# Kernel optimization log

Measured on AMD Instinct MI355X. Metric: run time of the kernel, lower is better.

## Reference

```python
import jax, jax.numpy as jnp
import numpy as np

N_NODES = 50000
N_EDGES = 800000
IN_FEATS = 128
OUT_FEATS = 128
HEADS = 2
EW_DIMS = 2
NEG_SLOPE = 0.2


def setup_inputs() -> dict:
    key = jax.random.key(0)
    ks = jax.random.split(key, 8)
    feat = jax.random.normal(ks[0], (N_NODES, IN_FEATS), dtype=jnp.float32)
    e_w = jax.random.uniform(ks[1], (N_EDGES, EW_DIMS), dtype=jnp.float32)
    src = jax.random.randint(ks[2], (N_EDGES,), 0, N_NODES)
    dst = jax.random.randint(ks[3], (N_EDGES,), 0, N_NODES)
    # Learned params: per-head fc weight, attn vectors (xavier-ish scale)
    s = 1.0 / np.sqrt(IN_FEATS)
    W = jax.random.normal(ks[4], (HEADS, OUT_FEATS, IN_FEATS), dtype=jnp.float32) * s
    attn_l = jax.random.normal(ks[5], (HEADS, OUT_FEATS), dtype=jnp.float32) * s
    attn_r = jax.random.normal(ks[6], (HEADS, OUT_FEATS), dtype=jnp.float32) * s
    attn_ew = jax.random.normal(ks[7], (HEADS, EW_DIMS), dtype=jnp.float32)
    return {"feat": feat, "e_w": e_w, "src": src, "dst": dst,
            "W": W, "attn_l": attn_l, "attn_r": attn_r, "attn_ew": attn_ew}


def reference(feat, e_w, src, dst, W, attn_l, attn_r, attn_ew):
    N = feat.shape[0]
    # per-head projection: [N, H, O]
    ft = jnp.einsum('nf,hof->nho', feat, W)
    el = jnp.einsum('nho,ho->nh', ft, attn_l)           # [N, H]
    er = jnp.einsum('nho,ho->nh', ft, attn_r)           # [N, H]
    ew = jnp.einsum('ed,hd->eh', e_w, attn_ew)          # [E, H]
    # u_add_v + edge-weight attention + leaky_relu
    e = jax.nn.leaky_relu(el[src] + er[dst] + ew, NEG_SLOPE)  # [E, H]
    # edge_softmax grouped by destination node (numerically stable)
    emax = jax.ops.segment_max(e, dst, num_segments=N)
    emax = jnp.where(jnp.isfinite(emax), emax, 0.0)
    ee = jnp.exp(e - emax[dst])
    denom = jax.ops.segment_sum(ee, dst, num_segments=N)
    a = ee / jnp.where(denom[dst] > 0, denom[dst], 1.0)       # [E, H]
    # u_mul_e / sum aggregation: [N, H, O]
    m = ft[src] * a[:, :, None]
    rst = jax.ops.segment_sum(m, dst, num_segments=N)
    # residual (Identity since in_feats == out_feats) + elu, then cat heads
    rst = jax.nn.elu(rst + feat[:, None, :])
    return rst.reshape(N, -1)
```

## Files before the change

### kernel.cpp

```cpp
#include <hip/hip_runtime.h>
#include <hip/hip_bf16.h>
#include <math.h>

#define NNODES 50000
#define NEDGES 800000
#define INF 128
#define OUTF 128
#define HEADS 2
#define NEG_SLOPE 0.2f

#define CAP 32
#define OVFCAP 32768

__device__ __forceinline__ unsigned short f2bf(float f) {
    unsigned u = __float_as_uint(f);
    unsigned r = (u + 0x7FFFu + ((u >> 16) & 1u)) >> 16;
    return (unsigned short)r;
}
__device__ __forceinline__ float bf2f(unsigned short b) {
    return __uint_as_float((unsigned)b << 16);
}

typedef __attribute__((ext_vector_type(8))) short frag_ab;
typedef __attribute__((ext_vector_type(4))) float frag_cd;

#define APITCH 136

__global__ void init_kernel(int* cursor, int* ovfcnt, int N) {
    int i = blockIdx.x * 256 + threadIdx.x;
    if (i < N) cursor[i] = 0;
    if (i == 0) *ovfcnt = 0;
}

__global__ __launch_bounds__(256) void gemm_mfma(const float* __restrict__ feat,
                                                 const float* __restrict__ W,
                                                 const float* __restrict__ attn_l,
                                                 const float* __restrict__ attn_r,
                                                 unsigned short* __restrict__ ftb,
                                                 float* __restrict__ elp,
                                                 float* __restrict__ erp,
                                                 int N) {
    __shared__ unsigned short Asl[64 * APITCH];
    __shared__ unsigned short Bsl[64 * APITCH];
    const int t = threadIdx.x;
    const int n0 = blockIdx.x * 64;
    const int w = t >> 6, lane = t & 63;
    const int m16 = lane & 15, quad = lane >> 4;

#pragma unroll
    for (int i = 0; i < 8; ++i) {
        int q = t + i * 256;
        int r = q >> 5;
        int c4 = q & 31;
        int gn = n0 + r;
        float4 g = (gn < N) ? *(const float4*)(feat + (size_t)gn * INF + c4 * 4)
                            : make_float4(0.f, 0.f, 0.f, 0.f);
        ushort4 v; v.x = f2bf(g.x); v.y = f2bf(g.y); v.z = f2bf(g.z); v.w = f2bf(g.w);
        *(ushort4*)(&Asl[r * APITCH + c4 * 4]) = v;
    }

    const int arow = w * 16 + m16;

    for (int jt = 0; jt < 4; ++jt) {
        __syncthreads();
#pragma unroll
        for (int i = 0; i < 8; ++i) {
            int q = t + i * 256;
            int r = q >> 5;
            int c4 = q & 31;
            float4 g = *(const float4*)(W + (size_t)(jt * 64 + r) * INF + c4 * 4);
            ushort4 v; v.x = f2bf(g.x); v.y = f2bf(g.y); v.z = f2bf(g.z); v.w = f2bf(g.w);
            *(ushort4*)(&Bsl[r * APITCH + c4 * 4]) = v;
        }
        __syncthreads();

        frag_cd acc[4];
#pragma unroll
        for (int nt = 0; nt < 4; ++nt) acc[nt] = frag_cd{0.f, 0.f, 0.f, 0.f};

#pragma unroll
        for (int kc = 0; kc < 4; ++kc) {
            frag_ab af = *(frag_ab*)(&Asl[arow * APITCH + kc * 32 + quad * 8]);
#pragma unroll
            for (int nt = 0; nt < 4; ++nt) {
                frag_ab bf = *(frag_ab*)(&Bsl[(nt * 16 + m16) * APITCH + kc * 32 + quad * 8]);
                acc[nt] = __builtin_amdgcn_mfma_f32_16x16x32_bf16(af, bf, acc[nt], 0, 0, 0);
            }
        }

        float pl[4] = {0.f, 0.f, 0.f, 0.f};
        float pr[4] = {0.f, 0.f, 0.f, 0.f};
#pragma unroll
        for (int nt = 0; nt < 4; ++nt) {
            int gj = jt * 64 + nt * 16 + m16;
            float a_l = attn_l[gj];
            float a_r = attn_r[gj];
#pragma unroll
            for (int reg = 0; reg < 4; ++reg) {
                float val = acc[nt][reg];
                pl[reg] += val * a_l;
                pr[reg] += val * a_r;
                int gm = n0 + w * 16 + quad * 4 + reg;
                if (gm < N)
                    ftb[(size_t)gm * 256 + gj] = f2bf(val);
            }
        }
#pragma unroll
        for (int m = 1; m < 16; m <<= 1) {
#pragma unroll
            for (int reg = 0; reg < 4; ++reg) {
                pl[reg] += __shfl_xor(pl[reg], m, 64);
                pr[reg] += __shfl_xor(pr[reg], m, 64);
            }
        }
        if (m16 == 0) {
#pragma unroll
            for (int reg = 0; reg < 4; ++reg) {
                int gm = n0 + w * 16 + quad * 4 + reg;
                if (gm < N) {
                    elp[(size_t)gm * 4 + jt] = pl[reg];
                    erp[(size_t)gm * 4 + jt] = pr[reg];
                }
            }
        }
    }
}

__global__ void edge_fused(const float* __restrict__ elp, const float* __restrict__ erp,
                           const float* __restrict__ e_w, const int* __restrict__ src,
                           const int* __restrict__ dst, const float* __restrict__ attn_ew,
                           int* __restrict__ cursor, int* __restrict__ ovfcnt,
                           uint2* __restrict__ edata, float4* __restrict__ ovf,
                           int E) {
    int e = blockIdx.x * 256 + threadIdx.x;
    if (e >= E) return;
    int s = src[e], d = dst[e];
    float2 ew2 = *(const float2*)(e_w + (size_t)e * 2);
    float4 elv = *(const float4*)(elp + (size_t)s * 4);
    float4 erv = *(const float4*)(erp + (size_t)d * 4);
    float v0 = (elv.x + elv.y) + (erv.x + erv.y) + ew2.x * attn_ew[0] + ew2.y * attn_ew[1];
    float v1 = (elv.z + elv.w) + (erv.z + erv.w) + ew2.x * attn_ew[2] + ew2.y * attn_ew[3];
    v0 = v0 >= 0.f ? v0 : NEG_SLOPE * v0;
    v1 = v1 >= 0.f ? v1 : NEG_SLOPE * v1;
    float ee0 = __expf(v0);
    float ee1 = __expf(v1);
    int pos = atomicAdd(cursor + d, 1);
    if (pos < CAP) {
        unsigned pk = ((unsigned)f2bf(ee1) << 16) | (unsigned)f2bf(ee0);
        edata[(size_t)d * CAP + pos] = make_uint2((unsigned)s, pk);
    } else {
        int o = atomicAdd(ovfcnt, 1);
        if (o < OVFCAP)
            ovf[o] = make_float4(__int_as_float(d), __int_as_float(s), ee0, ee1);
    }
}

__global__ __launch_bounds__(256) void aggregate(const unsigned short* __restrict__ ftb,
                                                 const float* __restrict__ feat,
                                                 const uint2* __restrict__ edata,
                                                 const int* __restrict__ cursor,
                                                 const int* __restrict__ ovfcnt,
                                                 const float4* __restrict__ ovf,
                                                 float* __restrict__ out, int N) {
    const int t = threadIdx.x;
    const int w = t >> 6, l = t & 63;
    const int n = blockIdx.x * 4 + w;
    if (n >= N) return;
    const int c0 = 4 * l;
    const int h = l >> 5;
    const int cnt = cursor[n];
    const int cmain = cnt < CAP ? cnt : CAP;
    const uint2* eb = edata + (size_t)n * CAP;

    float4 acc = make_float4(0.f, 0.f, 0.f, 0.f);
    float dn = 0.f;
#pragma unroll 4
    for (int i = 0; i < cmain; ++i) {
        uint2 rec = eb[i];
        int s = (int)rec.x;
        float a = bf2f((unsigned short)(h ? (rec.y >> 16) : (rec.y & 0xFFFFu)));
        dn += a;
        ushort4 v = *(const ushort4*)(ftb + (size_t)s * 256 + c0);
        acc.x += a * bf2f(v.x);
        acc.y += a * bf2f(v.y);
        acc.z += a * bf2f(v.z);
        acc.w += a * bf2f(v.w);
    }
    if (cnt > CAP) {
        int no = *ovfcnt; if (no > OVFCAP) no = OVFCAP;
        for (int i = 0; i < no; ++i) {
            float4 ov = ovf[i];
            if (__float_as_int(ov.x) == n) {
                int s = __float_as_int(ov.y);
                float a = h ? ov.w : ov.z;
                dn += a;
                ushort4 v = *(const ushort4*)(ftb + (size_t)s * 256 + c0);
                acc.x += a * bf2f(v.x);
                acc.y += a * bf2f(v.y);
                acc.z += a * bf2f(v.z);
                acc.w += a * bf2f(v.w);
            }
        }
    }
    float inv = dn > 0.f ? 1.0f / dn : 0.f;
    float4 f4 = *(const float4*)(feat + (size_t)n * INF + (c0 & 127));
    float4 r;
    r.x = acc.x * inv + f4.x;
    r.y = acc.y * inv + f4.y;
    r.z = acc.z * inv + f4.z;
    r.w = acc.w * inv + f4.w;
    r.x = r.x > 0.f ? r.x : expm1f(r.x);
    r.y = r.y > 0.f ? r.y : expm1f(r.y);
    r.z = r.z > 0.f ? r.z : expm1f(r.z);
    r.w = r.w > 0.f ? r.w : expm1f(r.w);
    *(float4*)(out + (size_t)n * 256 + c0) = r;
}

extern "C" void kernel_launch(void* const* d_in, const int* in_sizes, int n_in,
                              void* d_out, int out_size, void* d_ws, size_t ws_size,
                              hipStream_t stream) {
    const float* feat    = (const float*)d_in[0];
    const float* e_w     = (const float*)d_in[1];
    const int*   src     = (const int*)d_in[2];
    const int*   dst     = (const int*)d_in[3];
    const float* W       = (const float*)d_in[4];
    const float* attn_l  = (const float*)d_in[5];
    const float* attn_r  = (const float*)d_in[6];
    const float* attn_ew = (const float*)d_in[7];
    float* out = (float*)d_out;

    const int N = in_sizes[0] / INF;
    const int E = in_sizes[2];

    unsigned short* ftb = (unsigned short*)d_ws;
    uint2*  edata  = (uint2*)(ftb + (size_t)N * 256);
    float*  elp    = (float*)(edata + (size_t)N * CAP);
    float*  erp    = elp + (size_t)N * 4;
    float4* ovf    = (float4*)(erp + (size_t)N * 4);
    int*    cursor = (int*)(ovf + OVFCAP);
    int*    ovfcnt = cursor + N;

    init_kernel<<<(N + 255) / 256, 256, 0, stream>>>(cursor, ovfcnt, N);

    gemm_mfma<<<(N + 63) / 64, 256, 0, stream>>>(feat, W, attn_l, attn_r, ftb, elp, erp, N);

    edge_fused<<<(E + 255) / 256, 256, 0, stream>>>(elp, erp, e_w, src, dst, attn_ew,
                                                    cursor, ovfcnt, edata, ovf, E);

    aggregate<<<(N + 3) / 4, 256, 0, stream>>>(ftb, feat, edata, cursor, ovfcnt, ovf, out, N);
}
```

Baseline: 217.9 us.

## Fold attention vectors into weights, pre-convert W to bf16, coalesce ft stores

Computes el/er algebraically as feat·(attn^T W) in a new per-node kernel, with the folded vectors built in a prep kernel that also converts W to bf16 once and zeroes the cursors. The GEMM loads bf16 W directly and stages output tiles through LDS so ftb rows go out as wide coalesced stores instead of scattered 2-byte writes. The aggregate kernel loads each node's edge records once per lane and broadcasts them with shuffles, and unpacks bf16 with shifts and masks. This adds an extra kernel launch and an extra read of feat in exchange for less GEMM epilogue work and fewer uncoalesced stores.

```diff
diff --git a/kernel.cpp b/kernel.cpp
--- a/kernel.cpp
+++ b/kernel.cpp
@@ -23,22 +23,47 @@
 
 typedef __attribute__((ext_vector_type(8))) short frag_ab;
 typedef __attribute__((ext_vector_type(4))) float frag_cd;
+struct us8 { ushort4 a, b; };
 
 #define APITCH 136
-
-__global__ void init_kernel(int* cursor, int* ovfcnt, int N) {
-    int i = blockIdx.x * 256 + threadIdx.x;
+#define EPITCH 68
+
+__global__ __launch_bounds__(256) void prep(const float* __restrict__ W,
+                                            const float* __restrict__ attn_l,
+                                            const float* __restrict__ attn_r,
+                                            int* cursor, int* ovfcnt,
+                                            unsigned short* __restrict__ Wb,
+                                            float* __restrict__ wl, float* __restrict__ wr,
+                                            int N) {
+    const int b = blockIdx.x, t = threadIdx.x;
+    const int i = b * 256 + t;
     if (i < N) cursor[i] = 0;
     if (i == 0) *ovfcnt = 0;
+    if (b < 32) {
+        int idx = b * 256 + t;
+        float4 g = *(const float4*)(W + (size_t)idx * 4);
+        ushort4 v; v.x = f2bf(g.x); v.y = f2bf(g.y); v.z = f2bf(g.z); v.w = f2bf(g.w);
+        *(ushort4*)(Wb + (size_t)idx * 4) = v;
+    } else if (b == 32) {
+        int h = t >> 7, f = t & 127;
+        float s = 0.f;
+#pragma unroll 8
+        for (int o = 0; o < 128; ++o)
+            s += attn_l[h * 128 + o] * W[(size_t)(h * 128 + o) * 128 + f];
+        wl[t] = s;
+    } else if (b == 33) {
+        int h = t >> 7, f = t & 127;
+        float s = 0.f;
+#pragma unroll 8
+        for (int o = 0; o < 128; ++o)
+            s += attn_r[h * 128 + o] * W[(size_t)(h * 128 + o) * 128 + f];
+        wr[t] = s;
+    }
 }
 
 __global__ __launch_bounds__(256) void gemm_mfma(const float* __restrict__ feat,
-                                                 const float* __restrict__ W,
-                                                 const float* __restrict__ attn_l,
-                                                 const float* __restrict__ attn_r,
+                                                 const unsigned short* __restrict__ Wb,
                                                  unsigned short* __restrict__ ftb,
-                                                 float* __restrict__ elp,
-                                                 float* __restrict__ erp,
                                                  int N) {
     __shared__ unsigned short Asl[64 * APITCH];
     __shared__ unsigned short Bsl[64 * APITCH];
@@ -64,13 +89,12 @@
     for (int jt = 0; jt < 4; ++jt) {
         __syncthreads();
 #pragma unroll
-        for (int i = 0; i < 8; ++i) {
+        for (int i = 0; i < 4; ++i) {
             int q = t + i * 256;
-            int r = q >> 5;
-            int c4 = q & 31;
-            float4 g = *(const float4*)(W + (size_t)(jt * 64 + r) * INF + c4 * 4);
-            ushort4 v; v.x = f2bf(g.x); v.y = f2bf(g.y); v.z = f2bf(g.z); v.w = f2bf(g.w);
-            *(ushort4*)(&Bsl[r * APITCH + c4 * 4]) = v;
+            int r = q >> 4;
+            int c8 = q & 15;
+            us8 v = *(const us8*)(Wb + (size_t)(jt * 64 + r) * 128 + c8 * 8);
+            *(us8*)(&Bsl[r * APITCH + c8 * 8]) = v;
         }
         __syncthreads();
 
@@ -88,45 +112,58 @@
             }
         }
 
-        float pl[4] = {0.f, 0.f, 0.f, 0.f};
-        float pr[4] = {0.f, 0.f, 0.f, 0.f};
+        __syncthreads();
+        unsigned short* ep = &Bsl[w * 16 * EPITCH];
 #pragma unroll
         for (int nt = 0; nt < 4; ++nt) {
-            int gj = jt * 64 + nt * 16 + m16;
-            float a_l = attn_l[gj];
-            float a_r = attn_r[gj];
-#pragma unroll
-            for (int reg = 0; reg < 4; ++reg) {
-                float val = acc[nt][reg];
-                pl[reg] += val * a_l;
-                pr[reg] += val * a_r;
-                int gm = n0 + w * 16 + quad * 4 + reg;
-                if (gm < N)
-                    ftb[(size_t)gm * 256 + gj] = f2bf(val);
-            }
-        }
-#pragma unroll
-        for (int m = 1; m < 16; m <<= 1) {
-#pragma unroll
-            for (int reg = 0; reg < 4; ++reg) {
-                pl[reg] += __shfl_xor(pl[reg], m, 64);
-                pr[reg] += __shfl_xor(pr[reg], m, 64);
-            }
-        }
-        if (m16 == 0) {
-#pragma unroll
-            for (int reg = 0; reg < 4; ++reg) {
-                int gm = n0 + w * 16 + quad * 4 + reg;
-                if (gm < N) {
-                    elp[(size_t)gm * 4 + jt] = pl[reg];
-                    erp[(size_t)gm * 4 + jt] = pr[reg];
-                }
-            }
-        }
-    }
-}
-
-__global__ void edge_fused(const float* __restrict__ elp, const float* __restrict__ erp,
+#pragma unroll
+            for (int reg = 0; reg < 4; ++reg)
+                ep[(quad * 4 + reg) * EPITCH + nt * 16 + m16] = f2bf(acc[nt][reg]);
+        }
+        int r = lane >> 2;
+        int c = lane & 3;
+        us8 v0 = *(us8*)(&ep[r * EPITCH + c * 16]);
+        us8 v1 = *(us8*)(&ep[r * EPITCH + c * 16 + 8]);
+        int gm = n0 + w * 16 + r;
+        if (gm < N) {
+            *(us8*)(ftb + (size_t)gm * 256 + jt * 64 + c * 16) = v0;
+            *(us8*)(ftb + (size_t)gm * 256 + jt * 64 + c * 16 + 8) = v1;
+        }
+    }
+}
+
+__global__ __launch_bounds__(256) void eler_kernel(const float* __restrict__ feat,
+                                                   const float* __restrict__ wl,
+                                                   const float* __restrict__ wr,
+                                                   float2* __restrict__ el,
+                                                   float2* __restrict__ er, int N) {
+    __shared__ float swl[256], swr[256];
+    const int t = threadIdx.x;
+    swl[t] = wl[t];
+    swr[t] = wr[t];
+    __syncthreads();
+    const int w = t >> 6, lane = t & 63;
+    const int n = blockIdx.x * 4 + w;
+    if (n >= N) return;
+    float2 f = *(const float2*)(feat + (size_t)n * INF + lane * 2);
+    float l0 = f.x * swl[lane * 2] + f.y * swl[lane * 2 + 1];
+    float l1 = f.x * swl[128 + lane * 2] + f.y * swl[128 + lane * 2 + 1];
+    float r0 = f.x * swr[lane * 2] + f.y * swr[lane * 2 + 1];
+    float r1 = f.x * swr[128 + lane * 2] + f.y * swr[128 + lane * 2 + 1];
+#pragma unroll
+    for (int m = 1; m < 64; m <<= 1) {
+        l0 += __shfl_xor(l0, m, 64);
+        l1 += __shfl_xor(l1, m, 64);
+        r0 += __shfl_xor(r0, m, 64);
+        r1 += __shfl_xor(r1, m, 64);
+    }
+    if (lane == 0) {
+        el[n] = make_float2(l0, l1);
+        er[n] = make_float2(r0, r1);
+    }
+}
+
+__global__ void edge_fused(const float2* __restrict__ el, const float2* __restrict__ er,
                            const float* __restrict__ e_w, const int* __restrict__ src,
                            const int* __restrict__ dst, const float* __restrict__ attn_ew,
                            int* __restrict__ cursor, int* __restrict__ ovfcnt,
@@ -136,10 +173,10 @@
     if (e >= E) return;
     int s = src[e], d = dst[e];
     float2 ew2 = *(const float2*)(e_w + (size_t)e * 2);
-    float4 elv = *(const float4*)(elp + (size_t)s * 4);
-    float4 erv = *(const float4*)(erp + (size_t)d * 4);
-    float v0 = (elv.x + elv.y) + (erv.x + erv.y) + ew2.x * attn_ew[0] + ew2.y * attn_ew[1];
-    float v1 = (elv.z + elv.w) + (erv.z + erv.w) + ew2.x * attn_ew[2] + ew2.y * attn_ew[3];
+    float2 elv = el[s];
+    float2 erv = er[d];
+    float v0 = elv.x + erv.x + ew2.x * attn_ew[0] + ew2.y * attn_ew[1];
+    float v1 = elv.y + erv.y + ew2.x * attn_ew[2] + ew2.y * attn_ew[3];
     v0 = v0 >= 0.f ? v0 : NEG_SLOPE * v0;
     v1 = v1 >= 0.f ? v1 : NEG_SLOPE * v1;
     float ee0 = __expf(v0);
@@ -172,19 +209,21 @@
     const int cmain = cnt < CAP ? cnt : CAP;
     const uint2* eb = edata + (size_t)n * CAP;
 
+    uint2 myrec = (l < cmain) ? eb[l] : make_uint2(0u, 0u);
+
     float4 acc = make_float4(0.f, 0.f, 0.f, 0.f);
     float dn = 0.f;
 #pragma unroll 4
     for (int i = 0; i < cmain; ++i) {
-        uint2 rec = eb[i];
-        int s = (int)rec.x;
-        float a = bf2f((unsigned short)(h ? (rec.y >> 16) : (rec.y & 0xFFFFu)));
+        int s = __shfl((int)myrec.x, i, 64);
+        unsigned pk = (unsigned)__shfl((int)myrec.y, i, 64);
+        float a = __uint_as_float(h ? (pk & 0xFFFF0000u) : (pk << 16));
         dn += a;
-        ushort4 v = *(const ushort4*)(ftb + (size_t)s * 256 + c0);
-        acc.x += a * bf2f(v.x);
-        acc.y += a * bf2f(v.y);
-        acc.z += a * bf2f(v.z);
-        acc.w += a * bf2f(v.w);
+        uint2 v = *(const uint2*)(ftb + (size_t)s * 256 + c0);
+        acc.x += a * __uint_as_float(v.x << 16);
+        acc.y += a * __uint_as_float(v.x & 0xFFFF0000u);
+        acc.z += a * __uint_as_float(v.y << 16);
+        acc.w += a * __uint_as_float(v.y & 0xFFFF0000u);
     }
     if (cnt > CAP) {
         int no = *ovfcnt; if (no > OVFCAP) no = OVFCAP;
@@ -194,11 +233,11 @@
                 int s = __float_as_int(ov.y);
                 float a = h ? ov.w : ov.z;
                 dn += a;
-                ushort4 v = *(const ushort4*)(ftb + (size_t)s * 256 + c0);
-                acc.x += a * bf2f(v.x);
-                acc.y += a * bf2f(v.y);
-                acc.z += a * bf2f(v.z);
-                acc.w += a * bf2f(v.w);
+                uint2 v = *(const uint2*)(ftb + (size_t)s * 256 + c0);
+                acc.x += a * __uint_as_float(v.x << 16);
+                acc.y += a * __uint_as_float(v.x & 0xFFFF0000u);
+                acc.z += a * __uint_as_float(v.y << 16);
+                acc.w += a * __uint_as_float(v.y & 0xFFFF0000u);
             }
         }
     }
@@ -234,17 +273,23 @@
 
     unsigned short* ftb = (unsigned short*)d_ws;
     uint2*  edata  = (uint2*)(ftb + (size_t)N * 256);
-    float*  elp    = (float*)(edata + (size_t)N * CAP);
-    float*  erp    = elp + (size_t)N * 4;
-    float4* ovf    = (float4*)(erp + (size_t)N * 4);
+    float2* el     = (float2*)(edata + (size_t)N * CAP);
+    float2* er     = el + N;
+    unsigned short* Wb = (unsigned short*)(er + N);
+    float*  wl     = (float*)(Wb + 32768);
+    float*  wr     = wl + 256;
+    float4* ovf    = (float4*)(wr + 256);
     int*    cursor = (int*)(ovf + OVFCAP);
     int*    ovfcnt = cursor + N;
 
-    init_kernel<<<(N + 255) / 256, 256, 0, stream>>>(cursor, ovfcnt, N);
-
-    gemm_mfma<<<(N + 63) / 64, 256, 0, stream>>>(feat, W, attn_l, attn_r, ftb, elp, erp, N);
-
-    edge_fused<<<(E + 255) / 256, 256, 0, stream>>>(elp, erp, e_w, src, dst, attn_ew,
+    int pgrid = (N + 255) / 256; if (pgrid < 34) pgrid = 34;
+    prep<<<pgrid, 256, 0, stream>>>(W, attn_l, attn_r, cursor, ovfcnt, Wb, wl, wr, N);
+
+    gemm_mfma<<<(N + 63) / 64, 256, 0, stream>>>(feat, Wb, ftb, N);
+
+    eler_kernel<<<(N + 3) / 4, 256, 0, stream>>>(feat, wl, wr, el, er, N);
+
+    edge_fused<<<(E + 255) / 256, 256, 0, stream>>>(el, er, e_w, src, dst, attn_ew,
                                                     cursor, ovfcnt, edata, ovf, E);
 
     aggregate<<<(N + 3) / 4, 256, 0, stream>>>(ftb, feat, edata, cursor, ovfcnt, ovf, out, N);
```

Measured after the change: 248.2 us. 13.9% more time.
